# Optimization experiments

Measured on AMD Instinct MI355X. Metric: run time of the kernel, lower is better.

The kernel has to match this reference:

```python
import jax, jax.numpy as jnp
import numpy as np

N, K, FIN, FOUT = 50000, 32, 128, 128

def setup_inputs() -> dict:
    key = jax.random.key(0)
    k1, k2, k3 = jax.random.split(key, 3)
    x = jax.random.normal(k1, (N, FIN), dtype=jnp.float32)
    nbrs = jax.random.randint(k2, (N, K), 0, N)
    # nn.Linear weight init scale ~ 1/sqrt(fan_in)
    W = jax.random.normal(k3, (FIN, FOUT), dtype=jnp.float32) / np.sqrt(FIN).astype(np.float32)
    return {"x": x, "nbrs": nbrs, "W": W}

def reference(x, nbrs, W):
    # h = self.w(x)  (bias=False)
    h = x @ W                              # [N, FOUT]
    g = jnp.take(h, nbrs, axis=0)          # [N, K, FOUT] gather of neighbor features
    s = jnp.sort(g, axis=1)                # sort each neighbor list per feature
    k = nbrs.shape[1]
    # torch.median returns the lower median: sorted[(k-1)//2]
    return s[:, (k - 1) // 2, :]           # [N, FOUT]
```

## Files before the change

kernel.cpp:

```cpp
#include <hip/hip_runtime.h>

#define FIN 128
#define FOUT 128
#define KNB 32

typedef __attribute__((ext_vector_type(8))) short bf16x8;
typedef __attribute__((ext_vector_type(4))) float f32x4;

__global__ __launch_bounds__(256) void wf_stage(
    const float* __restrict__ W, unsigned* __restrict__ wf) {
  const int id = blockIdx.x * 256 + threadIdx.x;
  if (id >= 2048) return;
  const int lane = id & 63;
  const int kb = (id >> 6) & 3;
  const int ct = id >> 8;
  const int krow = kb * 32 + (lane >> 4) * 8;
  const int col = ct * 16 + (lane & 15);
  unsigned d[4];
  #pragma unroll
  for (int p = 0; p < 4; ++p) {
    const float lo = W[(krow + 2 * p) * FOUT + col];
    const float hi = W[(krow + 2 * p + 1) * FOUT + col];
    asm("v_cvt_pk_bf16_f32 %0, %1, %2" : "=v"(d[p]) : "v"(lo), "v"(hi));
  }
  uint4 q; q.x = d[0]; q.y = d[1]; q.z = d[2]; q.w = d[3];
  *(uint4*)(wf + (size_t)id * 4) = q;
}

__global__ __launch_bounds__(256) void gemm_mfma(
    const float* __restrict__ x, const unsigned* __restrict__ wf,
    unsigned* __restrict__ h, int n_rows) {
  const int t = threadIdx.x;
  const int wv = t >> 6;
  const int l = t & 63;
  const int row = blockIdx.x * 64 + wv * 16 + (l & 15);
  const int rsafe = min(row, n_rows - 1);
  const int kq = l >> 4;

  bf16x8 xf[4];
  #pragma unroll
  for (int kb = 0; kb < 4; ++kb) {
    const float* xp = x + (size_t)rsafe * FIN + kb * 32 + kq * 8;
    const float4 x0 = *(const float4*)(xp);
    const float4 x1 = *(const float4*)(xp + 4);
    union { unsigned u[4]; bf16x8 v; } pk;
    asm("v_cvt_pk_bf16_f32 %0, %1, %2" : "=v"(pk.u[0]) : "v"(x0.x), "v"(x0.y));
    asm("v_cvt_pk_bf16_f32 %0, %1, %2" : "=v"(pk.u[1]) : "v"(x0.z), "v"(x0.w));
    asm("v_cvt_pk_bf16_f32 %0, %1, %2" : "=v"(pk.u[2]) : "v"(x1.x), "v"(x1.y));
    asm("v_cvt_pk_bf16_f32 %0, %1, %2" : "=v"(pk.u[3]) : "v"(x1.z), "v"(x1.w));
    xf[kb] = pk.v;
  }

  #pragma unroll
  for (int ct = 0; ct < 8; ++ct) {
    f32x4 acc = {0.f, 0.f, 0.f, 0.f};
    #pragma unroll
    for (int kb = 0; kb < 4; ++kb) {
      union { uint4 q; bf16x8 v; } af;
      af.q = *(const uint4*)(wf + (size_t)((ct * 4 + kb) * 64 + l) * 4);
      acc = __builtin_amdgcn_mfma_f32_16x16x32_bf16(af.v, xf[kb], acc, 0, 0, 0);
    }
    if (row < n_rows) {
      unsigned p0, p1;
      asm("v_cvt_pkrtz_f16_f32 %0, %1, %2" : "=v"(p0) : "v"(acc[0]), "v"(acc[1]));
      asm("v_cvt_pkrtz_f16_f32 %0, %1, %2" : "=v"(p1) : "v"(acc[2]), "v"(acc[3]));
      uint2 st; st.x = p0; st.y = p1;
      *(uint2*)(h + (size_t)row * 64 + ct * 8 + kq * 2) = st;
    }
  }
}

__device__ __forceinline__ void ce(unsigned& a, unsigned& b) {
  unsigned mn, mx;
  asm("v_pk_min_f16 %0, %1, %2" : "=v"(mn) : "v"(a), "v"(b));
  asm("v_pk_max_f16 %0, %1, %2" : "=v"(mx) : "v"(a), "v"(b));
  a = mn; b = mx;
}

#define OEMS16(v, base)                                                        \
  _Pragma("unroll") for (int p = 1; p < 16; p <<= 1)                           \
  _Pragma("unroll") for (int k = p; k >= 1; k >>= 1)                           \
  _Pragma("unroll") for (int j = k & (p - 1); j + k < 16; j += 2 * k)          \
  _Pragma("unroll") for (int i = 0; i < k; ++i)                                \
    if (((i + j) / (2 * p)) == ((i + j + k) / (2 * p)))                        \
      ce(v[(base) + i + j], v[(base) + i + j + k]);

__global__ __launch_bounds__(256) void median_gather(
    const unsigned* __restrict__ h, const int* __restrict__ nbrs,
    float* __restrict__ out, int n_nodes) {
  const int t = threadIdx.x;
  const int lane = t & 63;
  const int node = __builtin_amdgcn_readfirstlane(blockIdx.x * 4 + (t >> 6));
  const int* __restrict__ idx = nbrs + node * KNB;

  unsigned v[KNB];
  #pragma unroll
  for (int k = 0; k < KNB; ++k)
    v[k] = h[(unsigned)idx[k] * 64u + (unsigned)lane];

  OEMS16(v, 0)
  OEMS16(v, 16)

  unsigned m[16];
  #pragma unroll
  for (int i = 0; i < 16; ++i)
    asm("v_pk_min_f16 %0, %1, %2" : "=v"(m[i]) : "v"(v[i]), "v"(v[16 + 15 - i]));
  #pragma unroll
  for (int s = 8; s >= 1; s >>= 1)
    #pragma unroll
    for (int i = 0; i < s; ++i)
      asm("v_pk_max_f16 %0, %1, %2" : "=v"(m[i]) : "v"(m[i]), "v"(m[i + s]));

  float flo, fhi;
  asm("v_cvt_f32_f16 %0, %1" : "=v"(flo) : "v"(m[0]));
  asm("v_cvt_f32_f16 %0, %1" : "=v"(fhi) : "v"(m[0] >> 16));
  float2 o; o.x = flo; o.y = fhi;
  *(float2*)(out + (size_t)node * FOUT + lane * 2) = o;
}

extern "C" void kernel_launch(void* const* d_in, const int* in_sizes, int n_in,
                              void* d_out, int out_size, void* d_ws, size_t ws_size,
                              hipStream_t stream) {
  const float* x    = (const float*)d_in[0];
  const int*   nbrs = (const int*)d_in[1];
  const float* W    = (const float*)d_in[2];
  float* out = (float*)d_out;

  unsigned* h  = (unsigned*)d_ws;
  unsigned* wf = (unsigned*)d_ws + 3200000;

  const int n = in_sizes[0] / FIN;

  wf_stage<<<8, 256, 0, stream>>>(W, wf);
  gemm_mfma<<<(n + 63) / 64, 256, 0, stream>>>(x, wf, h, n);
  median_gather<<<n / 4, 256, 0, stream>>>(h, nbrs, out, n);
}
```

Measured before the change: 69.52 us.

## Split h into four column-quarter planes and gather per quarter for locality

The GEMM now writes h as four planes of 32 fp16 features per node (64B rows), with each wave owning one quarter of output columns and keeping its W fragments in registers across two 16-row tiles. The median kernel processes one quarter per block, staging neighbor indices in shared memory and letting 16 threads per node each gather 64B rows. The goal is for the gather working set per pass to fit better in cache (each plane is a quarter of h) and to avoid reloading W fragments. In exchange, nbrs is read four times, each gathered row is a smaller 64B segment, and more blocks are launched.

```diff
diff --git a/kernel.cpp b/kernel.cpp
--- a/kernel.cpp
+++ b/kernel.cpp
@@ -3,6 +3,7 @@
 #define FIN 128
 #define FOUT 128
 #define KNB 32
+#define QD 16
 
 typedef __attribute__((ext_vector_type(8))) short bf16x8;
 typedef __attribute__((ext_vector_type(4))) float f32x4;
@@ -31,41 +32,53 @@
     const float* __restrict__ x, const unsigned* __restrict__ wf,
     unsigned* __restrict__ h, int n_rows) {
   const int t = threadIdx.x;
-  const int wv = t >> 6;
+  const int w = t >> 6;
   const int l = t & 63;
-  const int row = blockIdx.x * 64 + wv * 16 + (l & 15);
-  const int rsafe = min(row, n_rows - 1);
   const int kq = l >> 4;
+  const int row_base = blockIdx.x * 32;
 
-  bf16x8 xf[4];
+  uint4 wfr[2][4];
   #pragma unroll
-  for (int kb = 0; kb < 4; ++kb) {
-    const float* xp = x + (size_t)rsafe * FIN + kb * 32 + kq * 8;
-    const float4 x0 = *(const float4*)(xp);
-    const float4 x1 = *(const float4*)(xp + 4);
-    union { unsigned u[4]; bf16x8 v; } pk;
-    asm("v_cvt_pk_bf16_f32 %0, %1, %2" : "=v"(pk.u[0]) : "v"(x0.x), "v"(x0.y));
-    asm("v_cvt_pk_bf16_f32 %0, %1, %2" : "=v"(pk.u[1]) : "v"(x0.z), "v"(x0.w));
-    asm("v_cvt_pk_bf16_f32 %0, %1, %2" : "=v"(pk.u[2]) : "v"(x1.x), "v"(x1.y));
-    asm("v_cvt_pk_bf16_f32 %0, %1, %2" : "=v"(pk.u[3]) : "v"(x1.z), "v"(x1.w));
-    xf[kb] = pk.v;
-  }
+  for (int c = 0; c < 2; ++c)
+    #pragma unroll
+    for (int kb = 0; kb < 4; ++kb)
+      wfr[c][kb] = *(const uint4*)(wf + (size_t)(((2 * w + c) * 4 + kb) * 64 + l) * 4);
 
   #pragma unroll
-  for (int ct = 0; ct < 8; ++ct) {
-    f32x4 acc = {0.f, 0.f, 0.f, 0.f};
+  for (int tile = 0; tile < 2; ++tile) {
+    const int row = row_base + tile * 16 + (l & 15);
+    const int rsafe = min(row, n_rows - 1);
+
+    bf16x8 xf[4];
     #pragma unroll
     for (int kb = 0; kb < 4; ++kb) {
-      union { uint4 q; bf16x8 v; } af;
-      af.q = *(const uint4*)(wf + (size_t)((ct * 4 + kb) * 64 + l) * 4);
-      acc = __builtin_amdgcn_mfma_f32_16x16x32_bf16(af.v, xf[kb], acc, 0, 0, 0);
+      const float* xp = x + (size_t)rsafe * FIN + kb * 32 + kq * 8;
+      const float4 x0 = *(const float4*)(xp);
+      const float4 x1 = *(const float4*)(xp + 4);
+      union { unsigned u[4]; bf16x8 v; } pk;
+      asm("v_cvt_pk_bf16_f32 %0, %1, %2" : "=v"(pk.u[0]) : "v"(x0.x), "v"(x0.y));
+      asm("v_cvt_pk_bf16_f32 %0, %1, %2" : "=v"(pk.u[1]) : "v"(x0.z), "v"(x0.w));
+      asm("v_cvt_pk_bf16_f32 %0, %1, %2" : "=v"(pk.u[2]) : "v"(x1.x), "v"(x1.y));
+      asm("v_cvt_pk_bf16_f32 %0, %1, %2" : "=v"(pk.u[3]) : "v"(x1.z), "v"(x1.w));
+      xf[kb] = pk.v;
     }
-    if (row < n_rows) {
-      unsigned p0, p1;
-      asm("v_cvt_pkrtz_f16_f32 %0, %1, %2" : "=v"(p0) : "v"(acc[0]), "v"(acc[1]));
-      asm("v_cvt_pkrtz_f16_f32 %0, %1, %2" : "=v"(p1) : "v"(acc[2]), "v"(acc[3]));
-      uint2 st; st.x = p0; st.y = p1;
-      *(uint2*)(h + (size_t)row * 64 + ct * 8 + kq * 2) = st;
+
+    #pragma unroll
+    for (int c = 0; c < 2; ++c) {
+      f32x4 acc = {0.f, 0.f, 0.f, 0.f};
+      #pragma unroll
+      for (int kb = 0; kb < 4; ++kb) {
+        union { uint4 q; bf16x8 v; } af;
+        af.q = wfr[c][kb];
+        acc = __builtin_amdgcn_mfma_f32_16x16x32_bf16(af.v, xf[kb], acc, 0, 0, 0);
+      }
+      if (row < n_rows) {
+        unsigned p0, p1;
+        asm("v_cvt_pkrtz_f16_f32 %0, %1, %2" : "=v"(p0) : "v"(acc[0]), "v"(acc[1]));
+        asm("v_cvt_pkrtz_f16_f32 %0, %1, %2" : "=v"(p1) : "v"(acc[2]), "v"(acc[3]));
+        uint2 st; st.x = p0; st.y = p1;
+        *(uint2*)(h + ((size_t)w * n_rows + row) * QD + c * 8 + kq * 2) = st;
+      }
     }
   }
 }
@@ -75,6 +88,16 @@
   asm("v_pk_min_f16 %0, %1, %2" : "=v"(mn) : "v"(a), "v"(b));
   asm("v_pk_max_f16 %0, %1, %2" : "=v"(mx) : "v"(a), "v"(b));
   a = mn; b = mx;
+}
+__device__ __forceinline__ unsigned pmin(unsigned a, unsigned b) {
+  unsigned r;
+  asm("v_pk_min_f16 %0, %1, %2" : "=v"(r) : "v"(a), "v"(b));
+  return r;
+}
+__device__ __forceinline__ unsigned pmax(unsigned a, unsigned b) {
+  unsigned r;
+  asm("v_pk_max_f16 %0, %1, %2" : "=v"(r) : "v"(a), "v"(b));
+  return r;
 }
 
 #define OEMS16(v, base)                                                        \
@@ -87,35 +110,53 @@
 
 __global__ __launch_bounds__(256) void median_gather(
     const unsigned* __restrict__ h, const int* __restrict__ nbrs,
-    float* __restrict__ out, int n_nodes) {
+    float* __restrict__ out, int n_nodes, int blocks_per_q) {
+  __shared__ int sidx[16 * 33];
   const int t = threadIdx.x;
-  const int lane = t & 63;
-  const int node = __builtin_amdgcn_readfirstlane(blockIdx.x * 4 + (t >> 6));
-  const int* __restrict__ idx = nbrs + node * KNB;
+  const int q  = blockIdx.x / blocks_per_q;
+  const int bq = blockIdx.x - q * blocks_per_q;
+  const int node_base = bq * 16;
+
+  {
+    const int2 p2 = *(const int2*)(nbrs + (size_t)node_base * KNB + t * 2);
+    const int e = t * 2;
+    const int nl0 = e >> 5, k0 = e & 31;
+    sidx[nl0 * 33 + k0] = p2.x;
+    sidx[nl0 * 33 + k0 + 1] = p2.y;
+  }
+  __syncthreads();
+
+  const int nl = t >> 4;
+  const int d  = t & 15;
+  const unsigned qbase = (unsigned)q * (unsigned)n_nodes * QD + (unsigned)d;
+
+  int idxv[KNB];
+  #pragma unroll
+  for (int k = 0; k < KNB; ++k) idxv[k] = sidx[nl * 33 + k];
 
   unsigned v[KNB];
   #pragma unroll
   for (int k = 0; k < KNB; ++k)
-    v[k] = h[(unsigned)idx[k] * 64u + (unsigned)lane];
+    v[k] = h[qbase + (unsigned)idxv[k] * QD];
 
   OEMS16(v, 0)
   OEMS16(v, 16)
 
   unsigned m[16];
   #pragma unroll
-  for (int i = 0; i < 16; ++i)
-    asm("v_pk_min_f16 %0, %1, %2" : "=v"(m[i]) : "v"(v[i]), "v"(v[16 + 15 - i]));
+  for (int i = 0; i < 16; ++i) m[i] = pmin(v[i], v[31 - i]);
   #pragma unroll
   for (int s = 8; s >= 1; s >>= 1)
     #pragma unroll
-    for (int i = 0; i < s; ++i)
-      asm("v_pk_max_f16 %0, %1, %2" : "=v"(m[i]) : "v"(m[i]), "v"(m[i + s]));
+    for (int i = 0; i < s; ++i) m[i] = pmax(m[i], m[i + s]);
 
   float flo, fhi;
   asm("v_cvt_f32_f16 %0, %1" : "=v"(flo) : "v"(m[0]));
   asm("v_cvt_f32_f16 %0, %1" : "=v"(fhi) : "v"(m[0] >> 16));
   float2 o; o.x = flo; o.y = fhi;
-  *(float2*)(out + (size_t)node * FOUT + lane * 2) = o;
+
+  const int node = node_base + nl;
+  *(float2*)(out + (size_t)node * FOUT + q * 32 + d * 2) = o;
 }
 
 extern "C" void kernel_launch(void* const* d_in, const int* in_sizes, int n_in,
@@ -132,6 +173,7 @@
   const int n = in_sizes[0] / FIN;
 
   wf_stage<<<8, 256, 0, stream>>>(W, wf);
-  gemm_mfma<<<(n + 63) / 64, 256, 0, stream>>>(x, wf, h, n);
-  median_gather<<<n / 4, 256, 0, stream>>>(h, nbrs, out, n);
+  gemm_mfma<<<(n + 31) / 32, 256, 0, stream>>>(x, wf, h, n);
+  const int bpq = n / 16;
+  median_gather<<<4 * bpq, 256, 0, stream>>>(h, nbrs, out, n, bpq);
 }
```

Measured after the change: 69.92 us. No clear change (+0.6%).

## Split h into feature quarters for cache-local gathers; stage W and indices in LDS

Applied to the files above, without the earlier changes.

The GEMM output h is stored as four separate feature-quarter planes (32 features each, 64 bytes per row), and the median kernel processes one quarter per block group. Each thread now handles 4 features with 8-byte loads, which makes each gathered working set a quarter the size and more cache resident. Neighbor indices are staged in LDS per block, W fragments are staged in LDS in the GEMM, and launch bounds request higher occupancy. In exchange, the neighbor list is read four times and register use rises because each thread holds 64 values.

```diff
diff --git a/kernel.cpp b/kernel.cpp
--- a/kernel.cpp
+++ b/kernel.cpp
@@ -3,6 +3,7 @@
 #define FIN 128
 #define FOUT 128
 #define KNB 32
+#define QD 16
 
 typedef __attribute__((ext_vector_type(8))) short bf16x8;
 typedef __attribute__((ext_vector_type(4))) float f32x4;
@@ -30,12 +31,17 @@
 __global__ __launch_bounds__(256) void gemm_mfma(
     const float* __restrict__ x, const unsigned* __restrict__ wf,
     unsigned* __restrict__ h, int n_rows) {
+  __shared__ uint4 wls[2048];
   const int t = threadIdx.x;
-  const int wv = t >> 6;
+  #pragma unroll
+  for (int i = 0; i < 8; ++i)
+    wls[i * 256 + t] = ((const uint4*)wf)[i * 256 + t];
+  __syncthreads();
+
   const int l = t & 63;
-  const int row = blockIdx.x * 64 + wv * 16 + (l & 15);
+  const int kq = l >> 4;
+  const int row = blockIdx.x * 64 + (t >> 6) * 16 + (l & 15);
   const int rsafe = min(row, n_rows - 1);
-  const int kq = l >> 4;
 
   bf16x8 xf[4];
   #pragma unroll
@@ -57,7 +63,7 @@
     #pragma unroll
     for (int kb = 0; kb < 4; ++kb) {
       union { uint4 q; bf16x8 v; } af;
-      af.q = *(const uint4*)(wf + (size_t)((ct * 4 + kb) * 64 + l) * 4);
+      af.q = wls[(ct * 4 + kb) * 64 + l];
       acc = __builtin_amdgcn_mfma_f32_16x16x32_bf16(af.v, xf[kb], acc, 0, 0, 0);
     }
     if (row < n_rows) {
@@ -65,16 +71,21 @@
       asm("v_cvt_pkrtz_f16_f32 %0, %1, %2" : "=v"(p0) : "v"(acc[0]), "v"(acc[1]));
       asm("v_cvt_pkrtz_f16_f32 %0, %1, %2" : "=v"(p1) : "v"(acc[2]), "v"(acc[3]));
       uint2 st; st.x = p0; st.y = p1;
-      *(uint2*)(h + (size_t)row * 64 + ct * 8 + kq * 2) = st;
+      *(uint2*)(h + ((size_t)(ct >> 1) * n_rows + row) * QD + (ct & 1) * 8 + kq * 2) = st;
     }
   }
 }
 
-__device__ __forceinline__ void ce(unsigned& a, unsigned& b) {
-  unsigned mn, mx;
-  asm("v_pk_min_f16 %0, %1, %2" : "=v"(mn) : "v"(a), "v"(b));
-  asm("v_pk_max_f16 %0, %1, %2" : "=v"(mx) : "v"(a), "v"(b));
-  a = mn; b = mx;
+__device__ __forceinline__ unsigned pmin(unsigned a, unsigned b) {
+  unsigned r; asm("v_pk_min_f16 %0, %1, %2" : "=v"(r) : "v"(a), "v"(b)); return r;
+}
+__device__ __forceinline__ unsigned pmax(unsigned a, unsigned b) {
+  unsigned r; asm("v_pk_max_f16 %0, %1, %2" : "=v"(r) : "v"(a), "v"(b)); return r;
+}
+__device__ __forceinline__ void ce(uint2& a, uint2& b) {
+  const unsigned mnx = pmin(a.x, b.x), mxx = pmax(a.x, b.x);
+  const unsigned mny = pmin(a.y, b.y), mxy = pmax(a.y, b.y);
+  a.x = mnx; a.y = mny; b.x = mxx; b.y = mxy;
 }
 
 #define OEMS16(v, base)                                                        \
@@ -85,37 +96,67 @@
     if (((i + j) / (2 * p)) == ((i + j + k) / (2 * p)))                        \
       ce(v[(base) + i + j], v[(base) + i + j + k]);
 
-__global__ __launch_bounds__(256) void median_gather(
+__global__ __launch_bounds__(256, 4) void median_gather(
     const unsigned* __restrict__ h, const int* __restrict__ nbrs,
-    float* __restrict__ out, int n_nodes) {
+    float* __restrict__ out, int n_nodes, int blocks_per_q) {
+  __shared__ int sidx[32 * 33];
   const int t = threadIdx.x;
-  const int lane = t & 63;
-  const int node = __builtin_amdgcn_readfirstlane(blockIdx.x * 4 + (t >> 6));
-  const int* __restrict__ idx = nbrs + node * KNB;
+  const int q  = blockIdx.x / blocks_per_q;
+  const int bq = blockIdx.x - q * blocks_per_q;
+  const int node_base = bq * 32;
 
-  unsigned v[KNB];
+  {
+    const int e = t * 4;
+    const long long g = (long long)node_base * KNB + e;
+    int4 p4 = {0, 0, 0, 0};
+    if (g + 3 < (long long)n_nodes * KNB) p4 = *(const int4*)(nbrs + g);
+    const int nl0 = e >> 5, k0 = e & 31;
+    sidx[nl0 * 33 + k0 + 0] = p4.x;
+    sidx[nl0 * 33 + k0 + 1] = p4.y;
+    sidx[nl0 * 33 + k0 + 2] = p4.z;
+    sidx[nl0 * 33 + k0 + 3] = p4.w;
+  }
+  __syncthreads();
+
+  const int nl = t >> 3;
+  const int d  = t & 7;
+  const unsigned qbase = (unsigned)q * (unsigned)n_nodes * QD + (unsigned)d * 2u;
+
+  uint2 v[KNB];
   #pragma unroll
-  for (int k = 0; k < KNB; ++k)
-    v[k] = h[(unsigned)idx[k] * 64u + (unsigned)lane];
+  for (int k = 0; k < KNB; ++k) {
+    const unsigned idx = (unsigned)sidx[nl * 33 + k];
+    v[k] = *(const uint2*)(h + qbase + idx * QD);
+  }
+  __builtin_amdgcn_sched_barrier(0);
 
   OEMS16(v, 0)
   OEMS16(v, 16)
 
-  unsigned m[16];
+  uint2 m[16];
   #pragma unroll
-  for (int i = 0; i < 16; ++i)
-    asm("v_pk_min_f16 %0, %1, %2" : "=v"(m[i]) : "v"(v[i]), "v"(v[16 + 15 - i]));
+  for (int i = 0; i < 16; ++i) {
+    m[i].x = pmin(v[i].x, v[31 - i].x);
+    m[i].y = pmin(v[i].y, v[31 - i].y);
+  }
   #pragma unroll
   for (int s = 8; s >= 1; s >>= 1)
     #pragma unroll
-    for (int i = 0; i < s; ++i)
-      asm("v_pk_max_f16 %0, %1, %2" : "=v"(m[i]) : "v"(m[i]), "v"(m[i + s]));
+    for (int i = 0; i < s; ++i) {
+      m[i].x = pmax(m[i].x, m[i + s].x);
+      m[i].y = pmax(m[i].y, m[i + s].y);
+    }
 
-  float flo, fhi;
-  asm("v_cvt_f32_f16 %0, %1" : "=v"(flo) : "v"(m[0]));
-  asm("v_cvt_f32_f16 %0, %1" : "=v"(fhi) : "v"(m[0] >> 16));
-  float2 o; o.x = flo; o.y = fhi;
-  *(float2*)(out + (size_t)node * FOUT + lane * 2) = o;
+  float f0, f1, f2, f3;
+  asm("v_cvt_f32_f16 %0, %1" : "=v"(f0) : "v"(m[0].x));
+  asm("v_cvt_f32_f16 %0, %1" : "=v"(f1) : "v"(m[0].x >> 16));
+  asm("v_cvt_f32_f16 %0, %1" : "=v"(f2) : "v"(m[0].y));
+  asm("v_cvt_f32_f16 %0, %1" : "=v"(f3) : "v"(m[0].y >> 16));
+  float4 o; o.x = f0; o.y = f1; o.z = f2; o.w = f3;
+
+  const int node = node_base + nl;
+  if (node < n_nodes)
+    *(float4*)(out + (size_t)node * FOUT + q * 32 + d * 4) = o;
 }
 
 extern "C" void kernel_launch(void* const* d_in, const int* in_sizes, int n_in,
@@ -133,5 +174,6 @@
 
   wf_stage<<<8, 256, 0, stream>>>(W, wf);
   gemm_mfma<<<(n + 63) / 64, 256, 0, stream>>>(x, wf, h, n);
-  median_gather<<<n / 4, 256, 0, stream>>>(h, nbrs, out, n);
+  const int bpq = (n + 31) / 32;
+  median_gather<<<4 * bpq, 256, 0, stream>>>(h, nbrs, out, n, bpq);
 }
```

Measured after the change: 63.38 us. -8.8%, faster.
